# Performance work log

Measured on AMD Instinct MI355X. Metric: run time of the kernel, lower is better.

Reference implementation:

```python
import jax, jax.numpy as jnp
import numpy as np


def _conv3x3(x, w, b):
    # standard 3x3 conv, stride 1, pad 1, NCHW/OIHW
    out = jax.lax.conv_general_dilated(
        x, w, window_strides=(1, 1), padding=((1, 1), (1, 1)),
        dimension_numbers=('NCHW', 'OIHW', 'NCHW'))
    return out + b[None, :, None, None]


def _deform_conv3x3(x, offsets, w, b):
    # torchvision DeformConv2d, kernel 3x3, stride 1, pad 1, dilation 1,
    # conv groups == offset groups == OG, zero padding for out-of-bounds samples.
    B, C, H, W = x.shape
    K = 9  # 3x3 taps
    OG = offsets.shape[1] // (2 * K)
    Cg = C // OG
    # offsets layout: [B, OG*K*2, H, W] with 2 = (dy, dx)
    off = offsets.reshape(B, OG, K, 2, H, W)
    ky = (jnp.arange(K) // 3 - 1).astype(x.dtype).reshape(1, 1, K, 1, 1)
    kx = (jnp.arange(K) % 3 - 1).astype(x.dtype).reshape(1, 1, K, 1, 1)
    # sampling positions per output pixel and tap: [B, OG, K, H, W]
    py = off[:, :, :, 0] + ky + jnp.arange(H, dtype=x.dtype).reshape(1, 1, 1, H, 1)
    px = off[:, :, :, 1] + kx + jnp.arange(W, dtype=x.dtype).reshape(1, 1, 1, 1, W)
    y0 = jnp.floor(py)
    x0 = jnp.floor(px)
    x_g = x.reshape(B, OG, Cg, H * W)
    acc = jnp.zeros((B, OG, Cg, K, H, W), dtype=x.dtype)
    # bilinear interpolation: accumulate 4 corners, masking out-of-bounds to zero
    for yy, xx in ((y0, x0), (y0, x0 + 1), (y0 + 1, x0), (y0 + 1, x0 + 1)):
        wgt = (1.0 - jnp.abs(py - yy)) * (1.0 - jnp.abs(px - xx))
        valid = ((yy >= 0) & (yy < H) & (xx >= 0) & (xx < W)).astype(x.dtype)
        yi = jnp.clip(yy, 0, H - 1).astype(jnp.int32)
        xi = jnp.clip(xx, 0, W - 1).astype(jnp.int32)
        idx = (yi * W + xi).reshape(B, OG, 1, K * H * W)
        idx = jnp.broadcast_to(idx, (B, OG, Cg, K * H * W))
        vals = jnp.take_along_axis(x_g, idx, axis=-1).reshape(B, OG, Cg, K, H, W)
        acc = acc + vals * (wgt * valid)[:, :, None]
    # grouped conv over sampled patches: w is [C_out, C_in/OG, 3, 3]
    wk = w.reshape(OG, Cg, Cg, K)  # (group, out-per-group, in-per-group, tap)
    out = jnp.einsum('bgckhw,gock->bgohw', acc, wk).reshape(B, C, H, W)
    return out + b[None, :, None, None]


def setup_inputs() -> dict:
    key = jax.random.key(0)
    k0, k1, k2, k3 = jax.random.split(key, 4)
    B, C, H, W, OG = 8, 256, 64, 64, 4
    x = jax.random.normal(k0, (B, C, H, W), jnp.float32)
    # small offset-conv weights so predicted offsets stay in a realistic range
    w_off = jax.random.normal(k1, (2 * 9 * OG, C, 3, 3), jnp.float32) * 0.01
    b_off = jnp.zeros((2 * 9 * OG,), jnp.float32)
    fan_in = (C // OG) * 9
    w_def = jax.random.normal(k2, (C, C // OG, 3, 3), jnp.float32) * (1.0 / np.sqrt(fan_in))
    b_def = jax.random.normal(k3, (C,), jnp.float32) * 0.01
    return {"x": x, "w_off": w_off, "b_off": b_off, "w_def": w_def, "b_def": b_def}


def reference(x, w_off, b_off, w_def, b_def):
    offsets = _conv3x3(x, w_off, b_off)
    return _deform_conv3x3(x, offsets, w_def, b_def)
```

## Files before the change

### kernel.cpp

```cpp
#include <hip/hip_runtime.h>
#include <hip/hip_bf16.h>

#define BATCH 8
#define CIN   256
#define HH    64
#define WW    64
#define HW    4096
#define OG    4
#define CG    64
#define COFF  72

typedef __attribute__((ext_vector_type(8))) _Float16 half8;
typedef __attribute__((ext_vector_type(4))) float floatx4;

static __device__ __forceinline__ half8 splat8(float f) {
    _Float16 h = (_Float16)f;
    return (half8){h, h, h, h, h, h, h, h};
}

#define OFFS_ELEMS (BATCH * COFF * HH * WW)
#define WT_ELEMS   (OG * 9 * 4 * 2 * 64 * 8)
#define WO3_ELEMS  (8 * 9 * 5 * 64 * 8)
#define XH_BYTE_OFF ((size_t)OFFS_ELEMS * 4 + (size_t)WT_ELEMS * 2 + (size_t)WO3_ELEMS * 2)
#define NEED_NHWC (XH_BYTE_OFF + (size_t)BATCH * HW * CIN * 2)

#define PREPW_BLOCKS (((WT_ELEMS + WO3_ELEMS) + 255) / 256)

__global__ __launch_bounds__(256) void prep_kernel(
    const float* __restrict__ x, const float* __restrict__ w_def,
    const float* __restrict__ w_off, _Float16* __restrict__ xh,
    _Float16* __restrict__ wT3, _Float16* __restrict__ woT3)
{
    const int t = threadIdx.x;
    if (blockIdx.x >= 512) {
        int i = (blockIdx.x - 512) * 256 + t;
        if (i < WT_ELEMS) {
            int j = i & 7;
            int l = (i >> 3) & 63;
            int rest = i >> 9;
            int kh = rest & 1;
            int mt = (rest >> 1) & 3;
            int gk = rest >> 3;
            int k = gk % 9, g = gk / 9;
            int o = mt * 16 + (l & 15);
            int c = kh * 32 + (l >> 4) * 8 + j;
            wT3[i] = (_Float16)w_def[((size_t)((g * CG + o) * CG + c)) * 9 + k];
        } else if (i < WT_ELEMS + WO3_ELEMS) {
            int idx = i - WT_ELEMS;
            int j = idx & 7;
            int l = (idx >> 3) & 63;
            int rest = idx >> 9;
            int mt = rest % 5;
            int ct = rest / 5;
            int tap = ct % 9, chunk = ct / 9;
            int o = mt * 16 + (l & 15);
            int c = chunk * 32 + (l >> 4) * 8 + j;
            float v = (o < COFF) ? w_off[((size_t)(o * CIN + c)) * 9 + tap] : 0.f;
            woT3[idx] = (_Float16)v;
        }
        return;
    }

    const int b = blockIdx.x >> 6;
    const int y = blockIdx.x & 63;

    __shared__ short tile[64][258];

#pragma unroll
    for (int it = 0; it < 16; ++it) {
        int i  = t + it * 256;
        int c  = i >> 4;
        int p4 = (i & 15) << 2;
        float4 v = *(const float4*)(x + (((size_t)(b * CIN + c)) << 12) + (y << 6) + p4);
        tile[p4 + 0][c] = __builtin_bit_cast(short, (_Float16)v.x);
        tile[p4 + 1][c] = __builtin_bit_cast(short, (_Float16)v.y);
        tile[p4 + 2][c] = __builtin_bit_cast(short, (_Float16)v.z);
        tile[p4 + 3][c] = __builtin_bit_cast(short, (_Float16)v.w);
    }
    __syncthreads();

    _Float16* dst = xh + (((size_t)(b * HW)) << 8) + ((size_t)(y * WW) << 8);
#pragma unroll
    for (int k = 0; k < 8; ++k) {
        int i  = t + k * 256;
        int p  = i >> 5;
        int c8 = (i & 31) << 3;
        const unsigned* tp = (const unsigned*)&tile[p][c8];
        uint4 r = make_uint4(tp[0], tp[1], tp[2], tp[3]);
        *(uint4*)(dst + ((size_t)p << 8) + c8) = r;
    }
}

__global__ __launch_bounds__(512) void conv_off_nhwc(
    const _Float16* __restrict__ xh, const _Float16* __restrict__ woT3,
    const float* __restrict__ b_off, float* __restrict__ offs)
{
    const int b = blockIdx.x >> 6;
    const int h = blockIdx.x & 63;
    const int t = threadIdx.x;
    const int wv = t >> 6;
    const int l  = t & 63;
    const int lane16 = l & 15;
    const int quad   = l >> 4;
    const int pg = wv & 3;
    const int mh = wv >> 2;
    const int p  = pg * 16 + lane16;
    const int mt0 = mh ? 3 : 0;
    const int nmt = mh ? 2 : 3;

    __shared__ _Float16 xs[3][66][40];
    __shared__ _Float16 wa[45 * 512];

    floatx4 acc[3];
#pragma unroll
    for (int m = 0; m < 3; ++m) acc[m] = (floatx4){0.f, 0.f, 0.f, 0.f};

    if (t < 24) {
        int row = t >> 3;
        int rec = (t & 4) ? 65 : 0;
        int sub = t & 3;
        *(uint4*)&xs[row][rec][sub * 8] = make_uint4(0, 0, 0, 0);
    }

    uint4 ra[6], rb[2];
    auto issue = [&](int chunk) {
        const uint4* asrc = (const uint4*)(woT3 + (size_t)chunk * 45 * 512);
#pragma unroll
        for (int it = 0; it < 6; ++it) {
            int i = t + it * 512;
            ra[it] = (i < 2880) ? asrc[i] : make_uint4(0, 0, 0, 0);
        }
#pragma unroll
        for (int it = 0; it < 2; ++it) {
            int i = t + it * 512;
            int sub = i & 3, rec = (i >> 2) & 63, ky = i >> 8;
            int yy = h + ky - 1;
            uint4 v = make_uint4(0, 0, 0, 0);
            if (i < 768 && (unsigned)yy < 64u)
                v = *(const uint4*)(xh + (((size_t)(b * HW + (yy << 6) + rec)) << 8)
                                       + chunk * 32 + sub * 8);
            rb[it] = v;
        }
    };
    auto commit = [&]() {
#pragma unroll
        for (int it = 0; it < 6; ++it) {
            int i = t + it * 512;
            if (i < 2880) *(uint4*)&wa[i * 8] = ra[it];
        }
#pragma unroll
        for (int it = 0; it < 2; ++it) {
            int i = t + it * 512;
            if (i < 768) {
                int sub = i & 3, rec = (i >> 2) & 63, ky = i >> 8;
                *(uint4*)&xs[ky][rec + 1][sub * 8] = rb[it];
            }
        }
    };

    issue(0);
    commit();
    __syncthreads();

    for (int chunk = 0; chunk < 8; ++chunk) {
        if (chunk < 7) issue(chunk + 1);

#pragma unroll
        for (int tap = 0; tap < 9; ++tap) {
            const int ky = tap / 3, kx = tap % 3;
            half8 bfrag = *(const half8*)&xs[ky][p + kx][quad * 8];
            const _Float16* ab = wa + (size_t)(tap * 5 + mt0) * 512 + l * 8;
            for (int m = 0; m < nmt; ++m) {
                half8 afrag = *(const half8*)(ab + m * 512);
                acc[m] = __builtin_amdgcn_mfma_f32_16x16x32_f16(afrag, bfrag, acc[m], 0, 0, 0);
            }
        }

        if (chunk < 7) {
            __syncthreads();
            commit();
            __syncthreads();
        }
    }

    for (int m = 0; m < nmt; ++m) {
#pragma unroll
        for (int rg = 0; rg < 4; ++rg) {
            int oc = (mt0 + m) * 16 + quad * 4 + rg;
            if (oc < COFF)
                offs[((size_t)(b * COFF + oc) << 12) + (h << 6) + p] =
                    acc[m][rg] + b_off[oc];
        }
    }
}

__global__ __launch_bounds__(512) void deform_nhwc(
    const _Float16* __restrict__ xh, const float* __restrict__ offs,
    const _Float16* __restrict__ wT3, const float* __restrict__ b_def,
    float* __restrict__ out)
{
    const int hh = blockIdx.x & 31;
    const int bg = blockIdx.x >> 5;
    const int g  = bg & 3;
    const int b  = bg >> 2;
    const int h0 = hh << 1;
    const int t  = threadIdx.x;
    const int wv = t >> 6;
    const int l  = t & 63;
    const int lane16 = l & 15;
    const int quad   = l >> 4;
    const int p  = (wv & 3) * 16 + lane16;
    const int hw = h0 + (wv >> 2);

    __shared__ _Float16 ls[6 * 64 * 72];
    __shared__ _Float16 wa2[2][4096];

    floatx4 acc[4];
#pragma unroll
    for (int mt = 0; mt < 4; ++mt) acc[mt] = (floatx4){0.f, 0.f, 0.f, 0.f};

#pragma unroll
    for (int it = 0; it < 6; ++it) {
        int id  = it * 512 + t;
        int c16 = id & 7;
        int px  = (id >> 3) & 63;
        int r   = id >> 9;
        int r_img = h0 - 2 + r;
        uint4 v = make_uint4(0, 0, 0, 0);
        if ((unsigned)r_img < 64u)
            v = *(const uint4*)(xh + (((size_t)(b * HW + (r_img << 6) + px)) << 8)
                                   + g * 64 + c16 * 8);
        *(uint4*)&ls[(r * 64 + px) * 72 + c16 * 8] = v;
    }

    {
        const uint4* asrc = (const uint4*)(wT3 + ((size_t)(g * 9) << 12));
        uint4 a0 = asrc[t];
        *(uint4*)&wa2[0][t * 8] = a0;
    }

    float dyv[9], dxv[9];
    {
        const float* ofb = offs + (((size_t)(b * COFF + g * 18)) * HH + hw) * WW + p;
#pragma unroll
        for (int k = 0; k < 9; ++k) {
            dyv[k] = ofb[(size_t)(2 * k) * HW];
            dxv[k] = ofb[(size_t)(2 * k + 1) * HW];
        }
    }

    __syncthreads();

    const _Float16* xg = xh + (((size_t)(b * HW)) << 8) + g * 64;

#pragma unroll
    for (int k = 0; k < 9; ++k) {
        uint4 pw0;
        if (k < 8) {
            const uint4* asrc = (const uint4*)(wT3 + ((size_t)(g * 9 + k + 1) << 12));
            pw0 = asrc[t];
        }

        float py = dyv[k] + (float)(hw + (k / 3) - 1);
        float px_ = dxv[k] + (float)(p + (k % 3) - 1);
        float y0f = floorf(py), x0f = floorf(px_);
        float fy = py - y0f, fx = px_ - x0f;
        int y0 = (int)y0f, x0 = (int)x0f;
        float wy0 = ((y0 >= 0) & (y0 < HH)) ? (1.f - fy) : 0.f;
        float wy1 = ((y0 >= -1) & (y0 < HH - 1)) ? fy : 0.f;
        float wx0 = ((x0 >= 0) & (x0 < WW)) ? (1.f - fx) : 0.f;
        float wx1 = ((x0 >= -1) & (x0 < WW - 1)) ? fx : 0.f;
        int yia = min(max(y0, 0), HH - 1), yib = min(max(y0 + 1, 0), HH - 1);
        int xia = min(max(x0, 0), WW - 1), xib = min(max(x0 + 1, 0), WW - 1);
        bool inWin = (y0 >= h0 - 2) & (y0 <= h0 + 2);

        const int co = quad * 8;
        int wa_ = min(max(yia - (h0 - 2), 0), 5);
        int wb_ = min(max(yib - (h0 - 2), 0), 5);
        const _Float16* pa = ls + ((wa_ * 64 + xia) * 72);
        const _Float16* pb = ls + ((wa_ * 64 + xib) * 72);
        const _Float16* pc = ls + ((wb_ * 64 + xia) * 72);
        const _Float16* pd = ls + ((wb_ * 64 + xib) * 72);

        half8 aL = *(const half8*)(pa + co);
        half8 bL = *(const half8*)(pb + co);
        half8 cL = *(const half8*)(pc + co);
        half8 dL = *(const half8*)(pd + co);
        half8 aH = *(const half8*)(pa + co + 32);
        half8 bH = *(const half8*)(pb + co + 32);
        half8 cH = *(const half8*)(pc + co + 32);
        half8 dH = *(const half8*)(pd + co + 32);

        if (!inWin) {
            const _Float16* qa = xg + (((size_t)((yia << 6) + xia)) << 8);
            const _Float16* qb = xg + (((size_t)((yia << 6) + xib)) << 8);
            const _Float16* qc = xg + (((size_t)((yib << 6) + xia)) << 8);
            const _Float16* qd = xg + (((size_t)((yib << 6) + xib)) << 8);
            aL = *(const half8*)(qa + co);  aH = *(const half8*)(qa + co + 32);
            bL = *(const half8*)(qb + co);  bH = *(const half8*)(qb + co + 32);
            cL = *(const half8*)(qc + co);  cH = *(const half8*)(qc + co + 32);
            dL = *(const half8*)(qd + co);  dH = *(const half8*)(qd + co + 32);
        }

        half8 W00 = splat8(wy0 * wx0), W01 = splat8(wy0 * wx1);
        half8 W10 = splat8(wy1 * wx0), W11 = splat8(wy1 * wx1);
        half8 f0 = aL * W00 + bL * W01 + cL * W10 + dL * W11;
        half8 f1 = aH * W00 + bH * W01 + cH * W10 + dH * W11;

        const _Float16* wk = &wa2[k & 1][l * 8];
#pragma unroll
        for (int mt = 0; mt < 4; ++mt) {
            half8 a0 = *(const half8*)(wk + (mt * 2 + 0) * 512);
            half8 a1 = *(const half8*)(wk + (mt * 2 + 1) * 512);
            acc[mt] = __builtin_amdgcn_mfma_f32_16x16x32_f16(a0, f0, acc[mt], 0, 0, 0);
            acc[mt] = __builtin_amdgcn_mfma_f32_16x16x32_f16(a1, f1, acc[mt], 0, 0, 0);
        }

        if (k < 8) {
            *(uint4*)&wa2[(k + 1) & 1][t * 8] = pw0;
            __syncthreads();
        }
    }

#pragma unroll
    for (int mt = 0; mt < 4; ++mt) {
#pragma unroll
        for (int rg = 0; rg < 4; ++rg) {
            int o = mt * 16 + quad * 4 + rg;
            float v = acc[mt][rg] + b_def[g * CG + o];
            out[((size_t)(b * CIN + g * CG + o) * HH + hw) * WW + p] = v;
        }
    }
}

__global__ __launch_bounds__(256) void conv_off_fb(
    const float* __restrict__ x, const float* __restrict__ w_off,
    const float* __restrict__ b_off, float* __restrict__ offs)
{
    const int b = blockIdx.x >> 6;
    const int h = blockIdx.x & 63;
    const int t = threadIdx.x;
    const int w = t & 63;
    const int q = t >> 6;

    __shared__ float xsf[3][8][WW + 2];
    __shared__ float wtf[9][8][COFF];

    float acc[18];
#pragma unroll
    for (int j = 0; j < 18; ++j) acc[j] = 0.f;

    for (int c0 = 0; c0 < CIN; c0 += 8) {
        __syncthreads();
        for (int i = t; i < 3 * 8 * (WW + 2); i += 256) {
            int wp = i % (WW + 2);
            int rem = i / (WW + 2);
            int cc = rem % 8;
            int ky = rem / 8;
            int yy = h + ky - 1;
            int xx = wp - 1;
            float v = 0.f;
            if (yy >= 0 && yy < HH && xx >= 0 && xx < WW)
                v = x[(((size_t)b * CIN + c0 + cc) * HH + yy) * WW + xx];
            xsf[ky][cc][wp] = v;
        }
        for (int i = t; i < 9 * 8 * COFF; i += 256) {
            int oc = i % COFF;
            int rem = i / COFF;
            int cc = rem % 8;
            int tap = rem / 8;
            wtf[tap][cc][oc] = w_off[((size_t)oc * CIN + c0 + cc) * 9 + tap];
        }
        __syncthreads();
        for (int tap = 0; tap < 9; ++tap) {
            const int ky = tap / 3, kx = tap % 3;
#pragma unroll
            for (int cc = 0; cc < 8; ++cc) {
                float xv = xsf[ky][cc][w + kx];
#pragma unroll
                for (int j = 0; j < 18; ++j)
                    acc[j] += xv * wtf[tap][cc][q * 18 + j];
            }
        }
    }
#pragma unroll
    for (int j = 0; j < 18; ++j) {
        int oc = q * 18 + j;
        offs[(((size_t)b * COFF + oc) * HH + h) * WW + w] = acc[j] + b_off[oc];
    }
}

__global__ __launch_bounds__(256) void deform_fb(
    const float* __restrict__ x, const float* __restrict__ offs,
    const float* __restrict__ w_def, const float* __restrict__ b_def,
    float* __restrict__ out)
{
    const int h  = blockIdx.x & 63;
    const int bg = blockIdx.x >> 6;
    const int g  = bg & 3;
    const int b  = bg >> 2;
    const int t  = threadIdx.x;
    const int w  = t & 63;
    const int q  = t >> 6;

    __shared__ float vlds[CG][WW];
    __shared__ float wt2[CG][CG];
    __shared__ int   sidx[4][WW];
    __shared__ float swgt[4][WW];

    float acc[16];
#pragma unroll
    for (int j = 0; j < 16; ++j) acc[j] = 0.f;

    const float* xg = x + ((size_t)(b * CIN + g * CG)) * HW;

    for (int k = 0; k < 9; ++k) {
        __syncthreads();
        if (t < 64) {
            const int ky = k / 3 - 1, kx = k % 3 - 1;
            size_t obase = (((size_t)b * COFF + g * 18 + k * 2) * HH + h) * WW + w;
            float dy = offs[obase];
            float dx = offs[obase + (size_t)HW];
            float py = dy + (float)(h + ky);
            float px = dx + (float)(w + kx);
            float y0 = floorf(py), x0 = floorf(px);
            float fy = py - y0, fx = px - x0;
#pragma unroll
            for (int cn = 0; cn < 4; ++cn) {
                float yy = y0 + (float)(cn >> 1);
                float xx = x0 + (float)(cn & 1);
                float wy = (cn >> 1) ? fy : (1.f - fy);
                float wx = (cn & 1) ? fx : (1.f - fx);
                bool valid = (yy >= 0.f) && (yy < (float)HH) &&
                             (xx >= 0.f) && (xx < (float)WW);
                int yi = (int)fminf(fmaxf(yy, 0.f), (float)(HH - 1));
                int xi = (int)fminf(fmaxf(xx, 0.f), (float)(WW - 1));
                sidx[cn][w] = yi * WW + xi;
                swgt[cn][w] = valid ? (wy * wx) : 0.f;
            }
        }
        for (int i = t; i < CG * CG; i += 256) {
            int o = i >> 6, c = i & 63;
            wt2[c][o] = w_def[((size_t)(g * CG + o) * CG + c) * 9 + k];
        }
        __syncthreads();

        int   i0 = sidx[0][w], i1 = sidx[1][w], i2 = sidx[2][w], i3 = sidx[3][w];
        float g0 = swgt[0][w], g1 = swgt[1][w], g2 = swgt[2][w], g3 = swgt[3][w];
#pragma unroll
        for (int j = 0; j < 16; ++j) {
            int c = q * 16 + j;
            const float* xc = xg + (size_t)c * HW;
            float v = g0 * xc[i0] + g1 * xc[i1] + g2 * xc[i2] + g3 * xc[i3];
            vlds[c][w] = v;
        }
        __syncthreads();

#pragma unroll 4
        for (int c = 0; c < CG; ++c) {
            float xv = vlds[c][w];
#pragma unroll
            for (int j = 0; j < 16; ++j)
                acc[j] += xv * wt2[c][q * 16 + j];
        }
    }

#pragma unroll
    for (int j = 0; j < 16; ++j) {
        int o = q * 16 + j;
        out[(((size_t)b * CIN + g * CG + o) * HH + h) * WW + w] =
            acc[j] + b_def[g * CG + o];
    }
}

extern "C" void kernel_launch(void* const* d_in, const int* in_sizes, int n_in,
                              void* d_out, int out_size, void* d_ws, size_t ws_size,
                              hipStream_t stream) {
    const float* x     = (const float*)d_in[0];
    const float* w_off = (const float*)d_in[1];
    const float* b_off = (const float*)d_in[2];
    const float* w_def = (const float*)d_in[3];
    const float* b_def = (const float*)d_in[4];
    float* out = (float*)d_out;

    char* ws = (char*)d_ws;
    float*     offs = (float*)ws;
    _Float16*  wT3  = (_Float16*)(ws + (size_t)OFFS_ELEMS * 4);
    _Float16*  woT3 = (_Float16*)(ws + (size_t)OFFS_ELEMS * 4 + (size_t)WT_ELEMS * 2);
    _Float16*  xh   = (_Float16*)(ws + XH_BYTE_OFF);

    if (ws_size >= NEED_NHWC) {
        prep_kernel<<<512 + PREPW_BLOCKS, 256, 0, stream>>>(x, w_def, w_off, xh, wT3, woT3);
        conv_off_nhwc<<<BATCH * HH, 512, 0, stream>>>(xh, woT3, b_off, offs);
        deform_nhwc<<<BATCH * OG * 32, 512, 0, stream>>>(xh, offs, wT3, b_def, out);
    } else {
        conv_off_fb<<<BATCH * HH, 256, 0, stream>>>(x, w_off, b_off, offs);
        deform_fb<<<BATCH * OG * HH, 256, 0, stream>>>(x, offs, w_def, b_def, out);
    }
}
```

Baseline: 167.6 us.

## Restructure offset conv: two rows per block, split-K across waves, LDS reduction

The offset-conv kernel now handles two output rows per block and stages all 256 input channels for four input rows in LDS, using an XOR-swizzled layout to avoid bank conflicts. Each wave computes all five M tiles for four N fragments over a quarter of the channels, reading weights straight from global memory. Partial sums are then reduced through LDS before the store. This removes the per-chunk double-barrier pipeline and raises reuse of weight and input fragments. In exchange it uses a large LDS footprint (about 135KB) and many accumulator registers, halves the grid to 256 blocks, and relies on cache for the weight loads.

```diff
diff --git a/kernel.cpp b/kernel.cpp
--- a/kernel.cpp
+++ b/kernel.cpp
@@ -95,101 +95,115 @@
     const _Float16* __restrict__ xh, const _Float16* __restrict__ woT3,
     const float* __restrict__ b_off, float* __restrict__ offs)
 {
-    const int b = blockIdx.x >> 6;
-    const int h = blockIdx.x & 63;
-    const int t = threadIdx.x;
+    const int b  = blockIdx.x >> 5;
+    const int h0 = (blockIdx.x & 31) << 1;
+    const int t  = threadIdx.x;
     const int wv = t >> 6;
     const int l  = t & 63;
     const int lane16 = l & 15;
     const int quad   = l >> 4;
-    const int pg = wv & 3;
-    const int mh = wv >> 2;
-    const int p  = pg * 16 + lane16;
-    const int mt0 = mh ? 3 : 0;
-    const int nmt = mh ? 2 : 3;
-
-    __shared__ _Float16 xs[3][66][40];
-    __shared__ _Float16 wa[45 * 512];
-
-    floatx4 acc[3];
-#pragma unroll
-    for (int m = 0; m < 3; ++m) acc[m] = (floatx4){0.f, 0.f, 0.f, 0.f};
-
-    if (t < 24) {
-        int row = t >> 3;
-        int rec = (t & 4) ? 65 : 0;
-        int sub = t & 3;
-        *(uint4*)&xs[row][rec][sub * 8] = make_uint4(0, 0, 0, 0);
-    }
-
-    uint4 ra[6], rb[2];
-    auto issue = [&](int chunk) {
-        const uint4* asrc = (const uint4*)(woT3 + (size_t)chunk * 45 * 512);
-#pragma unroll
-        for (int it = 0; it < 6; ++it) {
-            int i = t + it * 512;
-            ra[it] = (i < 2880) ? asrc[i] : make_uint4(0, 0, 0, 0);
-        }
-#pragma unroll
-        for (int it = 0; it < 2; ++it) {
-            int i = t + it * 512;
-            int sub = i & 3, rec = (i >> 2) & 63, ky = i >> 8;
-            int yy = h + ky - 1;
-            uint4 v = make_uint4(0, 0, 0, 0);
-            if (i < 768 && (unsigned)yy < 64u)
-                v = *(const uint4*)(xh + (((size_t)(b * HW + (yy << 6) + rec)) << 8)
-                                       + chunk * 32 + sub * 8);
-            rb[it] = v;
-        }
-    };
-    auto commit = [&]() {
-#pragma unroll
-        for (int it = 0; it < 6; ++it) {
-            int i = t + it * 512;
-            if (i < 2880) *(uint4*)&wa[i * 8] = ra[it];
-        }
-#pragma unroll
-        for (int it = 0; it < 2; ++it) {
-            int i = t + it * 512;
-            if (i < 768) {
-                int sub = i & 3, rec = (i >> 2) & 63, ky = i >> 8;
-                *(uint4*)&xs[ky][rec + 1][sub * 8] = rb[it];
-            }
-        }
-    };
-
-    issue(0);
-    commit();
+    const int nh = wv & 1;
+    const int ks = wv >> 1;
+
+    __shared__ _Float16 xs[4][66][256];
+
+    floatx4 acc[5][4];
+#pragma unroll
+    for (int mt = 0; mt < 5; ++mt)
+#pragma unroll
+        for (int nf = 0; nf < 4; ++nf) acc[mt][nf] = (floatx4){0.f, 0.f, 0.f, 0.f};
+
+#pragma unroll
+    for (int i = 0; i < 16; ++i) {
+        int f    = (i << 9) + t;
+        int r    = f >> 11;
+        int px   = (f >> 5) & 63;
+        int slot = f & 31;
+        int yy   = h0 - 1 + r;
+        uint4 v = make_uint4(0, 0, 0, 0);
+        if ((unsigned)yy < 64u)
+            v = *(const uint4*)(xh + (((size_t)(b * HW + (yy << 6) + px)) << 8)
+                                   + (slot << 3));
+        int rec = px + 1;
+        *(uint4*)&xs[r][rec][(slot ^ (rec & 7)) << 3] = v;
+    }
+    if (t < 256) {
+        int r = t >> 6, side = (t >> 5) & 1, slot = t & 31;
+        int rec = side * 65;
+        *(uint4*)&xs[r][rec][(slot ^ (rec & 7)) << 3] = make_uint4(0, 0, 0, 0);
+    }
     __syncthreads();
 
-    for (int chunk = 0; chunk < 8; ++chunk) {
-        if (chunk < 7) issue(chunk + 1);
-
+#pragma unroll
+    for (int ch2 = 0; ch2 < 2; ++ch2) {
+        const int ch = ks * 2 + ch2;
 #pragma unroll
         for (int tap = 0; tap < 9; ++tap) {
             const int ky = tap / 3, kx = tap % 3;
-            half8 bfrag = *(const half8*)&xs[ky][p + kx][quad * 8];
-            const _Float16* ab = wa + (size_t)(tap * 5 + mt0) * 512 + l * 8;
-            for (int m = 0; m < nmt; ++m) {
-                half8 afrag = *(const half8*)(ab + m * 512);
-                acc[m] = __builtin_amdgcn_mfma_f32_16x16x32_f16(afrag, bfrag, acc[m], 0, 0, 0);
+
+            const _Float16* ab = woT3 + (((size_t)((ch * 9 + tap) * 5)) << 9) + (l << 3);
+            half8 a0 = *(const half8*)(ab);
+            half8 a1 = *(const half8*)(ab + 512);
+            half8 a2 = *(const half8*)(ab + 1024);
+            half8 a3 = *(const half8*)(ab + 1536);
+            half8 a4 = *(const half8*)(ab + 2048);
+
+            half8 bf[4];
+#pragma unroll
+            for (int nf = 0; nf < 4; ++nf) {
+                int rec  = nf * 16 + lane16 + kx;
+                int slot = (ch * 4 + quad) ^ (rec & 7);
+                bf[nf] = *(const half8*)&xs[nh + ky][rec][slot << 3];
             }
-        }
-
-        if (chunk < 7) {
-            __syncthreads();
-            commit();
-            __syncthreads();
-        }
-    }
-
-    for (int m = 0; m < nmt; ++m) {
-#pragma unroll
-        for (int rg = 0; rg < 4; ++rg) {
-            int oc = (mt0 + m) * 16 + quad * 4 + rg;
-            if (oc < COFF)
-                offs[((size_t)(b * COFF + oc) << 12) + (h << 6) + p] =
-                    acc[m][rg] + b_off[oc];
+
+#pragma unroll
+            for (int nf = 0; nf < 4; ++nf) {
+                acc[0][nf] = __builtin_amdgcn_mfma_f32_16x16x32_f16(a0, bf[nf], acc[0][nf], 0, 0, 0);
+                acc[1][nf] = __builtin_amdgcn_mfma_f32_16x16x32_f16(a1, bf[nf], acc[1][nf], 0, 0, 0);
+                acc[2][nf] = __builtin_amdgcn_mfma_f32_16x16x32_f16(a2, bf[nf], acc[2][nf], 0, 0, 0);
+                acc[3][nf] = __builtin_amdgcn_mfma_f32_16x16x32_f16(a3, bf[nf], acc[3][nf], 0, 0, 0);
+                acc[4][nf] = __builtin_amdgcn_mfma_f32_16x16x32_f16(a4, bf[nf], acc[4][nf], 0, 0, 0);
+            }
+        }
+    }
+
+    __syncthreads();
+    float* red = (float*)&xs[0][0][0];
+
+    if (ks != 0) {
+        float* dst = red + (size_t)(((ks - 1) * 2 + nh) * 5120) + (l << 2);
+#pragma unroll
+        for (int mt = 0; mt < 5; ++mt)
+#pragma unroll
+            for (int nf = 0; nf < 4; ++nf)
+                *(floatx4*)&dst[(mt * 4 + nf) * 256] = acc[mt][nf];
+    }
+    __syncthreads();
+
+    if (ks == 0) {
+#pragma unroll
+        for (int s = 0; s < 3; ++s) {
+            const float* src = red + (size_t)((s * 2 + nh) * 5120) + (l << 2);
+#pragma unroll
+            for (int mt = 0; mt < 5; ++mt)
+#pragma unroll
+                for (int nf = 0; nf < 4; ++nf)
+                    acc[mt][nf] += *(const floatx4*)&src[(mt * 4 + nf) * 256];
+        }
+        const int y = h0 + nh;
+#pragma unroll
+        for (int mt = 0; mt < 5; ++mt) {
+#pragma unroll
+            for (int rg = 0; rg < 4; ++rg) {
+                int oc = mt * 16 + quad * 4 + rg;
+                if (oc < COFF) {
+                    float bias = b_off[oc];
+#pragma unroll
+                    for (int nf = 0; nf < 4; ++nf)
+                        offs[(((size_t)(b * COFF + oc)) << 12) + (y << 6) + nf * 16 + lane16] =
+                            acc[mt][nf][rg] + bias;
+                }
+            }
         }
     }
 }
@@ -491,7 +505,7 @@
 
     if (ws_size >= NEED_NHWC) {
         prep_kernel<<<512 + PREPW_BLOCKS, 256, 0, stream>>>(x, w_def, w_off, xh, wT3, woT3);
-        conv_off_nhwc<<<BATCH * HH, 512, 0, stream>>>(xh, woT3, b_off, offs);
+        conv_off_nhwc<<<BATCH * 32, 512, 0, stream>>>(xh, woT3, b_off, offs);
         deform_nhwc<<<BATCH * OG * 32, 512, 0, stream>>>(xh, offs, wT3, b_def, out);
     } else {
         conv_off_fb<<<BATCH * HH, 256, 0, stream>>>(x, w_off, b_off, offs);
```

After: 141.7 us. 15.4% less time.
